# Kernel tuning notes

Hardware: AMD Instinct MI355X
Metric: run time of the kernel (lower is better)

## Reference

```python
import jax, jax.numpy as jnp
from jax import lax
import numpy as np

EPS = 1e-5

def _quant(w):
    # BitNet-style binarization: sign(w) scaled by mean(|w|), with STE (identity grad)
    alpha = jnp.mean(jnp.abs(w))
    wq = jnp.sign(w) * alpha
    return w + lax.stop_gradient(wq - w)

def _bn(x, gamma, beta, axes):
    mean = jnp.mean(x, axis=axes, keepdims=True)
    var = jnp.var(x, axis=axes, keepdims=True)
    shape = [1] * x.ndim
    shape[1] = x.shape[1]
    return (x - mean) * lax.rsqrt(var + EPS) * gamma.reshape(shape) + beta.reshape(shape)

def _conv(x, w):
    return lax.conv_general_dilated(x, w, window_strides=(1, 1), padding=((1, 1), (1, 1)),
                                    dimension_numbers=('NCHW', 'OIHW', 'NCHW'))

def _maxpool2(x):
    return lax.reduce_window(x, -jnp.inf, lax.max, (1, 1, 2, 2), (1, 1, 2, 2), 'VALID')

def setup_inputs() -> dict:
    key = jax.random.key(0)
    ks = jax.random.split(key, 5)
    return {
        'x': jax.random.normal(ks[0], (1024, 3, 32, 32), jnp.float32),
        'w1': jax.random.normal(ks[1], (64, 3, 3, 3), jnp.float32) * 0.1,
        'g1': jnp.ones((64,), jnp.float32), 'b1': jnp.zeros((64,), jnp.float32),
        'w2': jax.random.normal(ks[2], (128, 64, 3, 3), jnp.float32) * 0.05,
        'g2': jnp.ones((128,), jnp.float32), 'b2': jnp.zeros((128,), jnp.float32),
        'wfc1': jax.random.normal(ks[3], (256, 8192), jnp.float32) * 0.02,
        'g3': jnp.ones((256,), jnp.float32), 'b3': jnp.zeros((256,), jnp.float32),
        'wfc2': jax.random.normal(ks[4], (10, 256), jnp.float32) * 0.1,
    }

def reference(x, w1, g1, b1, w2, g2, b2, wfc1, g3, b3, wfc2):
    h = _conv(x, _quant(w1))                 # [B,64,32,32]
    h = _maxpool2(jax.nn.relu(_bn(h, g1, b1, (0, 2, 3))))  # [B,64,16,16]
    h = _conv(h, _quant(w2))                 # [B,128,16,16]
    h = _maxpool2(jax.nn.relu(_bn(h, g2, b2, (0, 2, 3))))  # [B,128,8,8]
    h = h.reshape(h.shape[0], -1)            # [B,8192]
    h = h @ _quant(wfc1).T                   # [B,256]
    h = jax.nn.relu(_bn(h, g3, b3, (0,)))
    return h @ _quant(wfc2).T                # [B,10]
```

## Files before the change

kernel.cpp:

```cpp
#include <hip/hip_runtime.h>
#include <stdint.h>

typedef unsigned short u16;
typedef unsigned int u32;
typedef __attribute__((ext_vector_type(8))) short s8v;
typedef __attribute__((ext_vector_type(4))) float f4v;
typedef __attribute__((ext_vector_type(8))) u16 u16x8;

__device__ __forceinline__ float bf2f(u16 u){
  union { u32 i; float f; } v; v.i = ((u32)u) << 16; return v.f;
}
__device__ __forceinline__ u16 f2bf(float f){
  union { float f; u32 i; } v; v.f = f;
  u32 i = v.i;
  return (u16)((i + 0x7fffu + ((i >> 16) & 1u)) >> 16);
}
__device__ __forceinline__ float sgnf(float w){
  return (w > 0.f) ? 1.f : ((w < 0.f) ? -1.f : 0.f);
}
__device__ __forceinline__ u16 sgn_bf(float w){
  return (w > 0.f) ? (u16)0x3F80 : ((w < 0.f) ? (u16)0xBF80 : (u16)0);
}

#define GLL16(gaddr, laddr) __builtin_amdgcn_global_load_lds( \
    (const __attribute__((address_space(1))) void*)(gaddr),   \
    (__attribute__((address_space(3))) void*)(laddr), 16, 0, 0)

__global__ __launch_bounds__(256) void k_signgen_small(const float* __restrict__ w1, const float* __restrict__ w2,
                                                       const float* __restrict__ wfc2,
                                                       u16* __restrict__ qw1b, u16* __restrict__ qw2b,
                                                       float* __restrict__ qwfc2, float* __restrict__ partials){
  int i = blockIdx.x * 256 + threadIdx.x;
  float av = 0.f; int slot;
  if (i < 73728){
    int j = i & 7, lane = (i >> 3) & 63, fid = i >> 9;
    int s = fid >> 4, ks = (fid >> 3) & 1, nt = fid & 7;
    int co = (lane & 15)*8 + nt;
    int c = ks*32 + (lane >> 4)*8 + j;
    float wv = w2[((size_t)co*64 + c)*9 + s];
    qw2b[i] = sgn_bf(wv);
    av = fabsf(wv); slot = 1;
  } else if (i < 73728 + 2048){
    int i3 = i - 73728;
    int j = i3 & 7, lane = (i3 >> 3) & 63, nt = i3 >> 9;
    int co = nt*16 + (lane & 15);
    int k = (lane >> 4)*8 + j;
    if (k < 27){
      float wv = w1[co*27 + k];
      qw1b[i3] = sgn_bf(wv);
      av = fabsf(wv);
    } else qw1b[i3] = (u16)0;
    slot = 0;
  } else {
    int i4 = i - (73728 + 2048);
    float wv = wfc2[i4];
    qwfc2[i4] = sgnf(wv);
    av = fabsf(wv); slot = 3;
  }
  #pragma unroll
  for (int off = 32; off > 0; off >>= 1) av += __shfl_xor(av, off);
  if ((threadIdx.x & 63) == 0) atomicAdd(partials + slot*256 + (blockIdx.x & 255), av);
}

__global__ __launch_bounds__(256) void k_fc1gen(const float* __restrict__ wfc1, u16* __restrict__ qfc1b,
                                                float* __restrict__ partials){
  __shared__ u16 tile[128*72];
  int co = blockIdx.x, t = threadIdx.x;
  const float4* src = (const float4*)(wfc1 + (size_t)co*8192);
  float av = 0.f;
  #pragma unroll
  for (int p = 0; p < 8; ++p){
    int k4 = t + p*256;
    float4 v = src[k4];
    int c = k4 >> 4, px = (k4 & 15)*4;
    u16* d = tile + c*72 + px;
    d[0] = sgn_bf(v.x); d[1] = sgn_bf(v.y); d[2] = sgn_bf(v.z); d[3] = sgn_bf(v.w);
    av += fabsf(v.x) + fabsf(v.y) + fabsf(v.z) + fabsf(v.w);
  }
  #pragma unroll
  for (int off = 32; off > 0; off >>= 1) av += __shfl_xor(av, off);
  if ((t & 63) == 0) atomicAdd(partials + 2*256 + (co & 255), av);
  __syncthreads();
  int co4 = co >> 4, co15 = co & 15;
  #pragma unroll
  for (int p = 0; p < 4; ++p){
    int m = t + p*256;
    int px = m >> 4, jj = m & 15;
    int kstep = px*4 + (jj >> 2), l16 = jj & 3;
    u16x8 o;
    #pragma unroll
    for (int u = 0; u < 8; ++u) o[u] = tile[(jj*8 + u)*72 + px];
    *(u16x8*)(qfc1b + ((size_t)(kstep*16 + co4)*512 + (l16*16 + co15)*8)) = o;
  }
}

__global__ void k_red4(const float* __restrict__ partials, float* __restrict__ absum){
  int t = threadIdx.x, w = t >> 6, lane = t & 63;
  const float* p = partials + w*256;
  float s = p[lane] + p[lane + 64] + p[lane + 128] + p[lane + 192];
  #pragma unroll
  for (int off = 32; off > 0; off >>= 1) s += __shfl_xor(s, off);
  if (lane == 0) absum[w] = s;
}

__global__ __launch_bounds__(256) void k_conv1m(const float* __restrict__ x, const u16* __restrict__ qw1b,
                                                const float* __restrict__ absum, u16* __restrict__ p1raw,
                                                float* __restrict__ gs, float* __restrict__ gq){
  __shared__ float xs[3*34*36];
  __shared__ __align__(16) u16 acol[256*40];
  __shared__ float ls1[64], ls2[64];
  int n = blockIdx.x, t = threadIdx.x;
  if (t < 64){ ls1[t] = 0.f; ls2[t] = 0.f; }
  for (int i = t; i < 3672; i += 256) xs[i] = 0.f;
  __syncthreads();
  const float4* xg = (const float4*)(x + (size_t)n * 3072);
  for (int i = t; i < 768; i += 256){
    float4 v = xg[i];
    int ci = i >> 8, rem = i & 255, y = rem >> 3, xq = (rem & 7) * 4;
    int base = ci*1224 + (y+1)*36 + 2 + xq;
    xs[base+0] = v.x; xs[base+1] = v.y; xs[base+2] = v.z; xs[base+3] = v.w;
  }
  int w = t >> 6, lane = t & 63, l15 = lane & 15, q = lane >> 4;
  const s8v* bp = (const s8v*)qw1b;
  s8v bf[4];
  #pragma unroll
  for (int nt = 0; nt < 4; ++nt) bf[nt] = bp[nt*64 + lane];
  float alpha = absum[0] * (1.f/1728.f);
  u16* p1img = p1raw + (size_t)n * 16384;
  float s1v[4], s2v[4];
  #pragma unroll
  for (int nt = 0; nt < 4; ++nt){ s1v[nt] = 0.f; s2v[nt] = 0.f; }
  for (int chunk = 0; chunk < 4; ++chunk){
    __syncthreads();
    {
      int mg = chunk*256 + t;
      int g = mg >> 2, s = mg & 3;
      int iy = 2*(g >> 4) + (s >> 1), ix = 2*(g & 15) + (s & 1);
      const float* xb = xs + iy*36 + ix + 1;
      u32 pk2[16];
      #pragma unroll
      for (int kk = 0; kk < 16; ++kk){
        int k0 = 2*kk, k1 = 2*kk + 1;
        u32 lo = (k0 < 27) ? (u32)f2bf(xb[(k0/9)*1224 + ((k0%9)/3)*36 + (k0%3)]) : 0u;
        u32 hi = (k1 < 27) ? (u32)f2bf(xb[(k1/9)*1224 + ((k1%9)/3)*36 + (k1%3)]) : 0u;
        pk2[kk] = lo | (hi << 16);
      }
      u32* ar = (u32*)(acol + t*40);
      #pragma unroll
      for (int v = 0; v < 4; ++v)
        *(uint4*)(ar + v*4) = make_uint4(pk2[v*4], pk2[v*4+1], pk2[v*4+2], pk2[v*4+3]);
    }
    __syncthreads();
    #pragma unroll
    for (int i = 0; i < 4; ++i){
      int tl = w*4 + i;
      s8v av = *(const s8v*)(acol + (tl*16 + l15)*40 + q*8);
      int g = chunk*64 + tl*4 + q;
      u16* drow = p1img + g*64 + l15;
      #pragma unroll
      for (int nt = 0; nt < 4; ++nt){
        f4v c = (f4v)(0.0f);
        c = __builtin_amdgcn_mfma_f32_16x16x32_bf16(av, bf[nt], c, 0, 0, 0);
        s1v[nt] += c[0] + c[1] + c[2] + c[3];
        s2v[nt] += c[0]*c[0] + c[1]*c[1] + c[2]*c[2] + c[3]*c[3];
        float pm = fmaxf(fmaxf(c[0], c[1]), fmaxf(c[2], c[3]));
        drow[nt*16] = f2bf(pm * alpha);
      }
    }
  }
  #pragma unroll
  for (int nt = 0; nt < 4; ++nt){
    s1v[nt] += __shfl_xor(s1v[nt], 16); s1v[nt] += __shfl_xor(s1v[nt], 32);
    s2v[nt] += __shfl_xor(s2v[nt], 16); s2v[nt] += __shfl_xor(s2v[nt], 32);
  }
  if (q == 0){
    #pragma unroll
    for (int nt = 0; nt < 4; ++nt){
      atomicAdd(&ls1[nt*16 + l15], s1v[nt]);
      atomicAdd(&ls2[nt*16 + l15], s2v[nt]);
    }
  }
  __syncthreads();
  if (t < 64){
    atomicAdd(gs + t, ls1[t] * alpha);
    atomicAdd(gq + t, ls2[t] * alpha * alpha);
  }
}

__global__ __launch_bounds__(256, 2) void k_conv2m(const u16* __restrict__ p1raw, const u16* __restrict__ qw2b,
                                                   const float* __restrict__ absum,
                                                   const float* __restrict__ s1, const float* __restrict__ q1,
                                                   const float* __restrict__ g1, const float* __restrict__ b1,
                                                   u16* __restrict__ p2raw,
                                                   float* __restrict__ gs, float* __restrict__ gq){
  __shared__ __align__(16) u16 img[16384];
  __shared__ __align__(16) u16 bstage[3][4096];
  int n = blockIdx.x, t = threadIdx.x;
  int c0 = (t & 7) * 8;
  float scv[8], biv[8];
  #pragma unroll
  for (int j = 0; j < 8; ++j){
    float m = s1[c0+j] * (1.f/1048576.f);
    float var = q1[c0+j] * (1.f/1048576.f) - m*m;
    float sc = g1[c0+j] * rsqrtf(var + 1e-5f);
    scv[j] = sc; biv[j] = b1[c0+j] - m*sc;
  }
  const u16* src = p1raw + (size_t)n * 16384;
  #pragma unroll
  for (int i = 0; i < 8; ++i){
    int id = i*256 + t;
    int px = id >> 3, unit = id & 7;
    int su = unit ^ (px & 7);
    u16x8 v = *(const u16x8*)(src + id*8);
    u16x8 o;
    #pragma unroll
    for (int j = 0; j < 8; ++j)
      o[j] = f2bf(fmaxf(bf2f(v[j]) * scv[j] + biv[j], 0.f));
    *(u16x8*)(img + px*64 + su*8) = o;
  }
  __syncthreads();
  int w = t >> 6, lane = t & 63, l15 = lane & 15, q = lane >> 4;
  const char* bsrc = (const char*)qw2b;
  {
    const char* g = bsrc + w*2048 + lane*16;
    char* l = ((char*)bstage[0]) + w*2048;
    GLL16(g, l); GLL16(g + 1024, l + 1024);
  }
  f4v acc[4][8];
  #pragma unroll
  for (int a = 0; a < 4; ++a)
    #pragma unroll
    for (int b = 0; b < 8; ++b) acc[a][b] = (f4v)(0.0f);
  #pragma unroll
  for (int dy = 0; dy < 3; ++dy){
    #pragma unroll
    for (int dx = 0; dx < 3; ++dx){
      int s = dy*3 + dx;
      int xv = l15 + dx - 1;
      bool vx = (xv >= 0) && (xv < 16);
      int xc = min(max(xv, 0), 15);
      #pragma unroll
      for (int ks = 0; ks < 2; ++ks){
        int p = s*2 + ks;
        if (p < 17){
          int pn = p + 1;
          const char* g = bsrc + pn*8192 + w*2048 + lane*16;
          char* l = ((char*)bstage[pn%3]) + w*2048;
          GLL16(g, l); GLL16(g + 1024, l + 1024);
          asm volatile("s_waitcnt vmcnt(2)" ::: "memory");
        } else {
          asm volatile("s_waitcnt vmcnt(0)" ::: "memory");
        }
        __builtin_amdgcn_s_barrier();
        asm volatile("" ::: "memory");
        const u16* bb = bstage[p%3];
        s8v bf[8];
        #pragma unroll
        for (int nt = 0; nt < 8; ++nt) bf[nt] = *(const s8v*)(bb + (nt*64 + lane)*8);
        __builtin_amdgcn_s_setprio(1);
        #pragma unroll
        for (int mt = 0; mt < 4; ++mt){
          int yv = w*4 + mt + dy - 1;
          if (yv < 0 || yv > 15) continue;
          int px = yv*16 + xc;
          int su = (ks*4 + q) ^ (px & 7);
          s8v av = *(const s8v*)(img + px*64 + su*8);
          if (!vx) av = (s8v)(short)0;
          #pragma unroll
          for (int nt = 0; nt < 8; ++nt)
            acc[mt][nt] = __builtin_amdgcn_mfma_f32_16x16x32_bf16(av, bf[nt], acc[mt][nt], 0, 0, 0);
        }
        __builtin_amdgcn_s_setprio(0);
      }
    }
  }
  float alpha = absum[1] * (1.f/73728.f);
  float s1v[8], s2v[8];
  #pragma unroll
  for (int nt = 0; nt < 8; ++nt){ s1v[nt] = 0.f; s2v[nt] = 0.f; }
  #pragma unroll
  for (int mp = 0; mp < 2; ++mp){
    #pragma unroll
    for (int rp = 0; rp < 2; ++rp){
      u16x8 pk;
      #pragma unroll
      for (int nt = 0; nt < 8; ++nt){
        float v0 = acc[2*mp][nt][2*rp]     * alpha;
        float v1 = acc[2*mp][nt][2*rp+1]   * alpha;
        float v2 = acc[2*mp+1][nt][2*rp]   * alpha;
        float v3 = acc[2*mp+1][nt][2*rp+1] * alpha;
        s1v[nt] += v0 + v1 + v2 + v3;
        s2v[nt] += v0*v0 + v1*v1 + v2*v2 + v3*v3;
        pk[nt] = f2bf(fmaxf(fmaxf(v0, v1), fmaxf(v2, v3)));
      }
      int opx = (w*2 + mp)*8 + (q*2 + rp);
      *(u16x8*)(p2raw + ((size_t)n*64 + opx)*128 + l15*8) = pk;
    }
  }
  #pragma unroll
  for (int nt = 0; nt < 8; ++nt){
    s1v[nt] += __shfl_xor(s1v[nt], 16); s1v[nt] += __shfl_xor(s1v[nt], 32);
    s2v[nt] += __shfl_xor(s2v[nt], 16); s2v[nt] += __shfl_xor(s2v[nt], 32);
  }
  __syncthreads();
  float* ls = (float*)img;
  if (t < 256) ls[t] = 0.f;
  __syncthreads();
  if (q == 0){
    #pragma unroll
    for (int nt = 0; nt < 8; ++nt){
      atomicAdd(&ls[l15*8 + nt], s1v[nt]);
      atomicAdd(&ls[128 + l15*8 + nt], s2v[nt]);
    }
  }
  __syncthreads();
  if (t < 128){ atomicAdd(gs + t, ls[t]); atomicAdd(gq + t, ls[128 + t]); }
}

__global__ __launch_bounds__(256) void k_bn2(u16* __restrict__ p2,
                                             const float* __restrict__ s2, const float* __restrict__ q2,
                                             const float* __restrict__ g2, const float* __restrict__ b2){
  size_t i = (size_t)blockIdx.x * 256 + threadIdx.x;
  int c0 = ((int)(i & 15)) * 8;
  float scv[8], biv[8];
  #pragma unroll
  for (int j = 0; j < 8; ++j){
    float m = s2[c0+j] * (1.f/262144.f);
    float var = q2[c0+j] * (1.f/262144.f) - m*m;
    float sc = g2[c0+j] * rsqrtf(var + 1e-5f);
    scv[j] = sc; biv[j] = b2[c0+j] - m*sc;
  }
  u16x8 v = *(u16x8*)(p2 + i*8);
  u16x8 o;
  #pragma unroll
  for (int j = 0; j < 8; ++j)
    o[j] = f2bf(fmaxf(bf2f(v[j]) * scv[j] + biv[j], 0.f));
  *(u16x8*)(p2 + i*8) = o;
}

__global__ __launch_bounds__(256) void k_fc1m(const u16* __restrict__ p2, const u16* __restrict__ qfc1b,
                                              const float* __restrict__ absum, float* __restrict__ h3p){
  int t = threadIdx.x;
  int bm = blockIdx.x, bn = blockIdx.y, kb = blockIdx.z;
  int w = t >> 6, lane = t & 63, l15 = lane & 15, q = lane >> 4;
  int rowbase = bm*128 + (w >> 1)*64;
  int ntb = bn*8 + (w & 1)*4;
  const s8v* bp = (const s8v*)qfc1b;
  f4v acc[4][4];
  #pragma unroll
  for (int a = 0; a < 4; ++a)
    #pragma unroll
    for (int b = 0; b < 4; ++b) acc[a][b] = (f4v)(0.0f);
  #pragma unroll 2
  for (int ks = 0; ks < 16; ++ks){
    int kst = kb*16 + ks;
    s8v bf[4], af[4];
    #pragma unroll
    for (int nt = 0; nt < 4; ++nt) bf[nt] = bp[(kst*16 + ntb + nt)*64 + lane];
    #pragma unroll
    for (int mt = 0; mt < 4; ++mt)
      af[mt] = *(const s8v*)(p2 + (size_t)(rowbase + mt*16 + l15)*8192 + kst*32 + q*8);
    #pragma unroll
    for (int mt = 0; mt < 4; ++mt)
      #pragma unroll
      for (int nt = 0; nt < 4; ++nt)
        acc[mt][nt] = __builtin_amdgcn_mfma_f32_16x16x32_bf16(af[mt], bf[nt], acc[mt][nt], 0, 0, 0);
  }
  float alpha = absum[2] * (1.f/2097152.f);
  float* dst = h3p + (size_t)kb * 262144;
  #pragma unroll
  for (int mt = 0; mt < 4; ++mt)
    #pragma unroll
    for (int nt = 0; nt < 4; ++nt){
      int col = (ntb + nt)*16 + l15;
      #pragma unroll
      for (int r = 0; r < 4; ++r)
        dst[(size_t)(rowbase + mt*16 + q*4 + r)*256 + col] = acc[mt][nt][r] * alpha;
    }
}

__global__ __launch_bounds__(256) void k_fin3f(const float* __restrict__ h3p, float* __restrict__ h3,
                                               float* __restrict__ s3, float* __restrict__ q3){
  int jb = blockIdx.x, ns = blockIdx.y, t = threadIdx.x;
  int jj = t & 31, nn = t >> 5;
  int j = jb*32 + jj;
  float s1 = 0.f, s2 = 0.f;
  for (int i = nn; i < 128; i += 8){
    int n = i*8 + ns;
    float v = 0.f;
    #pragma unroll 8
    for (int kb = 0; kb < 16; ++kb) v += h3p[(size_t)kb*262144 + n*256 + j];
    h3[n*256 + j] = v;
    s1 += v; s2 += v*v;
  }
  __shared__ float l1[256], l2[256];
  l1[t] = s1; l2[t] = s2;
  __syncthreads();
  if (t < 32){
    float a = 0.f, b = 0.f;
    #pragma unroll
    for (int k = 0; k < 8; ++k){ a += l1[t+32*k]; b += l2[t+32*k]; }
    atomicAdd(s3 + jb*32 + t, a); atomicAdd(q3 + jb*32 + t, b);
  }
}

__global__ __launch_bounds__(64) void k_fc2(const float* __restrict__ h3, const float* __restrict__ qwfc2,
                                            const float* __restrict__ absum,
                                            const float* __restrict__ s3, const float* __restrict__ q3,
                                            const float* __restrict__ g3, const float* __restrict__ b3,
                                            float* __restrict__ out){
  int n = blockIdx.x, lane = threadIdx.x;
  float a[4];
  #pragma unroll
  for (int i = 0; i < 4; ++i){
    int j = lane + 64*i;
    float m = s3[j] * (1.f/1024.f);
    float var = q3[j] * (1.f/1024.f) - m*m;
    float sc = g3[j] * rsqrtf(var + 1e-5f);
    float v = h3[(size_t)n*256 + j] * sc + (b3[j] - m*sc);
    a[i] = fmaxf(v, 0.f);
  }
  float alpha = absum[3] * (1.f/2560.f);
  #pragma unroll
  for (int k = 0; k < 10; ++k){
    float p = 0.f;
    #pragma unroll
    for (int i = 0; i < 4; ++i) p += a[i] * qwfc2[k*256 + lane + 64*i];
    #pragma unroll
    for (int off = 32; off > 0; off >>= 1) p += __shfl_down(p, off);
    if (lane == 0) out[n*10 + k] = p * alpha;
  }
}

extern "C" void kernel_launch(void* const* d_in, const int* in_sizes, int n_in,
                              void* d_out, int out_size, void* d_ws, size_t ws_size,
                              hipStream_t stream){
  (void)in_sizes; (void)n_in; (void)out_size; (void)ws_size;
  const float* x    = (const float*)d_in[0];
  const float* w1   = (const float*)d_in[1];
  const float* g1   = (const float*)d_in[2];
  const float* b1   = (const float*)d_in[3];
  const float* w2   = (const float*)d_in[4];
  const float* g2   = (const float*)d_in[5];
  const float* b2   = (const float*)d_in[6];
  const float* wfc1 = (const float*)d_in[7];
  const float* g3   = (const float*)d_in[8];
  const float* b3   = (const float*)d_in[9];
  const float* wfc2 = (const float*)d_in[10];
  float* out = (float*)d_out;

  float* wsf = (float*)d_ws;
  char*  wsb = (char*)d_ws;
  float* absum = wsf;
  float* s1 = wsf + 16;   float* q1 = wsf + 80;
  float* s2 = wsf + 144;  float* q2 = wsf + 272;
  float* s3 = wsf + 1024; float* q3 = wsf + 1280;
  float* partials = wsf + 2048;
  u16*   qw1b  = (u16*)(wsf + 4096);
  u16*   qw2b  = (u16*)(wsb + (64u << 10));
  float* qwfc2 = (float*)(wsb + (256u << 10));
  float* h3    = (float*)(wsb + (1ull << 20));
  u16*   qfc1b = (u16*)(wsb + (2ull << 20));
  u16*   p1t   = (u16*)(wsb + (8ull << 20) + 4096);
  u16*   p2    = (u16*)(wsb + (112ull << 20));
  float* h3p   = (float*)(wsb + (128ull << 20));

  hipMemsetAsync(wsf, 0, 3072 * sizeof(float), stream);
  k_signgen_small<<<306, 256, 0, stream>>>(w1, w2, wfc2, qw1b, qw2b, qwfc2, partials);
  k_fc1gen<<<256, 256, 0, stream>>>(wfc1, qfc1b, partials);
  k_red4<<<1, 256, 0, stream>>>(partials, absum);
  k_conv1m<<<1024, 256, 0, stream>>>(x, qw1b, absum, p1t, s1, q1);
  k_conv2m<<<1024, 256, 0, stream>>>(p1t, qw2b, absum, s1, q1, g1, b1, p2, s2, q2);
  k_bn2<<<4096, 256, 0, stream>>>(p2, s2, q2, g2, b2);
  k_fc1m<<<dim3(8, 2, 16), 256, 0, stream>>>(p2, qfc1b, absum, h3p);
  k_fin3f<<<dim3(8, 8), 256, 0, stream>>>(h3p, h3, s3, q3);
  k_fc2<<<1024, 64, 0, stream>>>(h3, qwfc2, absum, s3, q3, g3, b3, out);
}
```

Baseline: 237.3 us.

## Split conv2 output channels across 8 waves with 512-thread blocks

Conv2 blocks now have 512 threads (8 waves) instead of 256. Each wave covers 4 output rows and half of the 128 output channels, so the accumulator array shrinks from 32 to 16 tiles and register pressure drops. The per-stage weight prefetch is spread across more threads, and the stats reduction and output stores are adjusted to the channel halves. The goal is more waves in flight to hide LDS and MFMA latency. The cost is that each wave reloads the same A fragments, so per-block LDS read traffic roughly doubles, and the tap loop is no longer fully unrolled.

```diff
diff --git a/kernel.cpp b/kernel.cpp
--- a/kernel.cpp
+++ b/kernel.cpp
@@ -6,6 +6,7 @@
 typedef __attribute__((ext_vector_type(8))) short s8v;
 typedef __attribute__((ext_vector_type(4))) float f4v;
 typedef __attribute__((ext_vector_type(8))) u16 u16x8;
+typedef __attribute__((ext_vector_type(4))) u16 u16x4;
 
 __device__ __forceinline__ float bf2f(u16 u){
   union { u32 i; float f; } v; v.i = ((u32)u) << 16; return v.f;
@@ -187,7 +188,7 @@
   }
 }
 
-__global__ __launch_bounds__(256, 2) void k_conv2m(const u16* __restrict__ p1raw, const u16* __restrict__ qw2b,
+__global__ __launch_bounds__(512, 4) void k_conv2m(const u16* __restrict__ p1raw, const u16* __restrict__ qw2b,
                                                    const float* __restrict__ absum,
                                                    const float* __restrict__ s1, const float* __restrict__ q1,
                                                    const float* __restrict__ g1, const float* __restrict__ b1,
@@ -207,8 +208,8 @@
   }
   const u16* src = p1raw + (size_t)n * 16384;
   #pragma unroll
-  for (int i = 0; i < 8; ++i){
-    int id = i*256 + t;
+  for (int i = 0; i < 4; ++i){
+    int id = i*512 + t;
     int px = id >> 3, unit = id & 7;
     int su = unit ^ (px & 7);
     u16x8 v = *(const u16x8*)(src + id*8);
@@ -218,73 +219,67 @@
       o[j] = f2bf(fmaxf(bf2f(v[j]) * scv[j] + biv[j], 0.f));
     *(u16x8*)(img + px*64 + su*8) = o;
   }
-  __syncthreads();
   int w = t >> 6, lane = t & 63, l15 = lane & 15, q = lane >> 4;
+  int wr = w >> 1, wc = w & 1;
   const char* bsrc = (const char*)qw2b;
   {
-    const char* g = bsrc + w*2048 + lane*16;
-    char* l = ((char*)bstage[0]) + w*2048;
-    GLL16(g, l); GLL16(g + 1024, l + 1024);
-  }
-  f4v acc[4][8];
+    const char* g = bsrc + w*1024 + lane*16;
+    char* l = ((char*)bstage[0]) + w*1024;
+    GLL16(g, l);
+  }
+  __syncthreads();
+  f4v acc[4][4];
   #pragma unroll
   for (int a = 0; a < 4; ++a)
     #pragma unroll
-    for (int b = 0; b < 8; ++b) acc[a][b] = (f4v)(0.0f);
-  #pragma unroll
-  for (int dy = 0; dy < 3; ++dy){
-    #pragma unroll
-    for (int dx = 0; dx < 3; ++dx){
-      int s = dy*3 + dx;
-      int xv = l15 + dx - 1;
-      bool vx = (xv >= 0) && (xv < 16);
-      int xc = min(max(xv, 0), 15);
-      #pragma unroll
-      for (int ks = 0; ks < 2; ++ks){
-        int p = s*2 + ks;
-        if (p < 17){
-          int pn = p + 1;
-          const char* g = bsrc + pn*8192 + w*2048 + lane*16;
-          char* l = ((char*)bstage[pn%3]) + w*2048;
-          GLL16(g, l); GLL16(g + 1024, l + 1024);
-          asm volatile("s_waitcnt vmcnt(2)" ::: "memory");
-        } else {
-          asm volatile("s_waitcnt vmcnt(0)" ::: "memory");
-        }
-        __builtin_amdgcn_s_barrier();
-        asm volatile("" ::: "memory");
-        const u16* bb = bstage[p%3];
-        s8v bf[8];
+    for (int b = 0; b < 4; ++b) acc[a][b] = (f4v)(0.0f);
+  for (int p = 0; p < 18; ++p){
+    int s = p >> 1, ks = p & 1;
+    int dy = s / 3, dx = s - dy*3;
+    int xv = l15 + dx - 1;
+    bool vx = (xv >= 0) && (xv < 16);
+    int xc = min(max(xv, 0), 15);
+    if (p < 17){
+      const char* g = bsrc + (size_t)(p + 1)*8192 + w*1024 + lane*16;
+      char* l = ((char*)bstage[(p + 1) % 3]) + w*1024;
+      GLL16(g, l);
+      asm volatile("s_waitcnt vmcnt(1)" ::: "memory");
+    } else {
+      asm volatile("s_waitcnt vmcnt(0)" ::: "memory");
+    }
+    __builtin_amdgcn_s_barrier();
+    asm volatile("" ::: "memory");
+    const u16* bb = bstage[p % 3];
+    s8v bf[4];
+    #pragma unroll
+    for (int nt = 0; nt < 4; ++nt) bf[nt] = *(const s8v*)(bb + ((wc*4 + nt)*64 + lane)*8);
+    __builtin_amdgcn_s_setprio(1);
+    #pragma unroll
+    for (int mt = 0; mt < 4; ++mt){
+      int yv = wr*4 + mt + dy - 1;
+      if (yv >= 0 && yv <= 15){
+        int px = yv*16 + xc;
+        int su = (ks*4 + q) ^ (px & 7);
+        s8v av = *(const s8v*)(img + px*64 + su*8);
+        if (!vx) av = (s8v)(short)0;
         #pragma unroll
-        for (int nt = 0; nt < 8; ++nt) bf[nt] = *(const s8v*)(bb + (nt*64 + lane)*8);
-        __builtin_amdgcn_s_setprio(1);
-        #pragma unroll
-        for (int mt = 0; mt < 4; ++mt){
-          int yv = w*4 + mt + dy - 1;
-          if (yv < 0 || yv > 15) continue;
-          int px = yv*16 + xc;
-          int su = (ks*4 + q) ^ (px & 7);
-          s8v av = *(const s8v*)(img + px*64 + su*8);
-          if (!vx) av = (s8v)(short)0;
-          #pragma unroll
-          for (int nt = 0; nt < 8; ++nt)
-            acc[mt][nt] = __builtin_amdgcn_mfma_f32_16x16x32_bf16(av, bf[nt], acc[mt][nt], 0, 0, 0);
-        }
-        __builtin_amdgcn_s_setprio(0);
+        for (int nt = 0; nt < 4; ++nt)
+          acc[mt][nt] = __builtin_amdgcn_mfma_f32_16x16x32_bf16(av, bf[nt], acc[mt][nt], 0, 0, 0);
       }
     }
+    __builtin_amdgcn_s_setprio(0);
   }
   float alpha = absum[1] * (1.f/73728.f);
-  float s1v[8], s2v[8];
-  #pragma unroll
-  for (int nt = 0; nt < 8; ++nt){ s1v[nt] = 0.f; s2v[nt] = 0.f; }
+  float s1v[4], s2v[4];
+  #pragma unroll
+  for (int nt = 0; nt < 4; ++nt){ s1v[nt] = 0.f; s2v[nt] = 0.f; }
   #pragma unroll
   for (int mp = 0; mp < 2; ++mp){
     #pragma unroll
     for (int rp = 0; rp < 2; ++rp){
-      u16x8 pk;
-      #pragma unroll
-      for (int nt = 0; nt < 8; ++nt){
+      u16x4 pk;
+      #pragma unroll
+      for (int nt = 0; nt < 4; ++nt){
         float v0 = acc[2*mp][nt][2*rp]     * alpha;
         float v1 = acc[2*mp][nt][2*rp+1]   * alpha;
         float v2 = acc[2*mp+1][nt][2*rp]   * alpha;
@@ -293,12 +288,12 @@
         s2v[nt] += v0*v0 + v1*v1 + v2*v2 + v3*v3;
         pk[nt] = f2bf(fmaxf(fmaxf(v0, v1), fmaxf(v2, v3)));
       }
-      int opx = (w*2 + mp)*8 + (q*2 + rp);
-      *(u16x8*)(p2raw + ((size_t)n*64 + opx)*128 + l15*8) = pk;
-    }
-  }
-  #pragma unroll
-  for (int nt = 0; nt < 8; ++nt){
+      int opx = (wr*2 + mp)*8 + (q*2 + rp);
+      *(u16x4*)(p2raw + ((size_t)n*64 + opx)*128 + l15*8 + wc*4) = pk;
+    }
+  }
+  #pragma unroll
+  for (int nt = 0; nt < 4; ++nt){
     s1v[nt] += __shfl_xor(s1v[nt], 16); s1v[nt] += __shfl_xor(s1v[nt], 32);
     s2v[nt] += __shfl_xor(s2v[nt], 16); s2v[nt] += __shfl_xor(s2v[nt], 32);
   }
@@ -308,9 +303,9 @@
   __syncthreads();
   if (q == 0){
     #pragma unroll
-    for (int nt = 0; nt < 8; ++nt){
-      atomicAdd(&ls[l15*8 + nt], s1v[nt]);
-      atomicAdd(&ls[128 + l15*8 + nt], s2v[nt]);
+    for (int nt = 0; nt < 4; ++nt){
+      atomicAdd(&ls[l15*8 + wc*4 + nt], s1v[nt]);
+      atomicAdd(&ls[128 + l15*8 + wc*4 + nt], s2v[nt]);
     }
   }
   __syncthreads();
@@ -470,7 +465,7 @@
   k_fc1gen<<<256, 256, 0, stream>>>(wfc1, qfc1b, partials);
   k_red4<<<1, 256, 0, stream>>>(partials, absum);
   k_conv1m<<<1024, 256, 0, stream>>>(x, qw1b, absum, p1t, s1, q1);
-  k_conv2m<<<1024, 256, 0, stream>>>(p1t, qw2b, absum, s1, q1, g1, b1, p2, s2, q2);
+  k_conv2m<<<1024, 512, 0, stream>>>(p1t, qw2b, absum, s1, q1, g1, b1, p2, s2, q2);
   k_bn2<<<4096, 256, 0, stream>>>(p2, s2, q2, g2, b2);
   k_fc1m<<<dim3(8, 2, 16), 256, 0, stream>>>(p2, qfc1b, absum, h3p);
   k_fin3f<<<dim3(8, 8), 256, 0, stream>>>(h3p, h3, s3, q3);
```

Measured after the change: 235.5 us. No clear change (-0.7%).
